# Optimization experiments

Hardware: AMD Instinct MI355X
Metric: run time of the kernel (lower is better)

The kernel has to match this reference:

```python
import jax, jax.numpy as jnp
import numpy as np

H, KVH, HD, D, FF = 16, 4, 128, 2048, 7168
EPS = 1e-5
ROPE_THETA = 10000.0
SCALE_FACTOR, SCALE_GAP = 1.0, 0.7


def rms_norm(x, w):
    v = jnp.mean(jnp.square(x.astype(jnp.float32)), axis=-1, keepdims=True)
    return (x.astype(jnp.float32) * jax.lax.rsqrt(v + EPS)).astype(x.dtype) * w


def apply_rope(x, pos):
    # x: [B,S,h,HD], pos: [S]
    inv = 1.0 / (ROPE_THETA ** (jnp.arange(0, HD, 2, dtype=jnp.float32) / HD))
    ang = pos.astype(jnp.float32)[:, None] * inv[None, :]              # [S,HD/2]
    cos = jnp.concatenate([jnp.cos(ang)] * 2, -1)[None, :, None, :]    # [1,S,1,HD]
    sin = jnp.concatenate([jnp.sin(ang)] * 2, -1)[None, :, None, :]
    x1, x2 = jnp.split(x, 2, axis=-1)
    rot = jnp.concatenate([-x2, x1], axis=-1)
    return x * cos + rot * sin


def attention(x, q_w, k_w, v_w, o_w):
    B, S, _ = x.shape
    pos = jnp.arange(S)
    q = apply_rope((x @ q_w.T).reshape(B, S, H, HD), pos)
    k = apply_rope((x @ k_w.T).reshape(B, S, KVH, HD), pos)
    v = (x @ v_w.T).reshape(B, S, KVH, HD)
    rep = H // KVH
    k = jnp.repeat(k, rep, axis=2)   # [B,S,H,HD]
    v = jnp.repeat(v, rep, axis=2)
    scores = jnp.einsum('bqhd,bkhd->bhqk', q, k) / np.sqrt(HD).astype(np.float32)
    causal = jnp.tril(jnp.ones((S, S), dtype=bool))
    scores = jnp.where(causal[None, None], scores, jnp.finfo(scores.dtype).min)
    probs = jax.nn.softmax(scores, axis=-1)
    out = jnp.einsum('bhqk,bkhd->bqhd', probs, v).reshape(B, S, H * HD)
    return out @ o_w.T


def mlp(x, gate_w, up_w, down_w):
    return (jax.nn.silu(x @ gate_w.T) * (x @ up_w.T)) @ down_w.T


def setup_inputs() -> dict:
    key = jax.random.key(0)
    ks = jax.random.split(key, 12)
    B, S = 2, 2048
    w = lambda k, shp: (jax.random.normal(k, shp, dtype=jnp.float32) * 0.02)
    return {
        'hidden_states': jax.random.normal(ks[0], (B, S, D), dtype=jnp.float32),
        'topk_mask': jax.random.randint(ks[1], (B, S), 0, 2) > 0,
        'topk_scores': jax.random.uniform(ks[2], (B, S), dtype=jnp.float32),
        'ln1_w': jnp.ones((D,), jnp.float32),
        'ln2_w': jnp.ones((D,), jnp.float32),
        'q_w': w(ks[3], (H * HD, D)),
        'k_w': w(ks[4], (KVH * HD, D)),
        'v_w': w(ks[5], (KVH * HD, D)),
        'o_w': w(ks[6], (D, H * HD)),
        'gate_w': w(ks[7], (FF, D)),
        'up_w': w(ks[8], (FF, D)),
        'down_w': w(ks[9], (D, FF)),
    }


def reference(hidden_states, topk_mask, topk_scores, ln1_w, ln2_w,
              q_w, k_w, v_w, o_w, gate_w, up_w, down_w):
    # attention block
    h = hidden_states + attention(rms_norm(hidden_states, ln1_w), q_w, k_w, v_w, o_w)
    # MoD top-k masked MLP: only selected tokens go through MLP, scaled, scattered back
    m = mlp(rms_norm(h, ln2_w), gate_w, up_w, down_w)
    scores = 0.5 * SCALE_FACTOR + (topk_scores - 0.5) * SCALE_GAP
    upd = jnp.where(topk_mask[..., None], m * scores[..., None], 0.0)
    return h + upd
```

## Files before the change

kernel.cpp:

```cpp
#include <hip/hip_runtime.h>
#include <stdint.h>

#define SEQ    2048
#define DMODEL 2048
#define NTOK   4096
#define NHEAD  16
#define NKVH   4
#define HDIM   128
#define FFDIM  7168
#define FFH    3584
#define QKVS   3072

typedef __bf16 bf16x8 __attribute__((ext_vector_type(8)));
typedef float  floatx4 __attribute__((ext_vector_type(4)));

__device__ __forceinline__ float bf2f(unsigned short u) {
  union { unsigned int i; float f; } v; v.i = ((unsigned int)u) << 16; return v.f;
}
__device__ __forceinline__ unsigned short f2bf(float f) {
  union { float f; unsigned int u; } v; v.f = f;
  unsigned int r = (v.u + 0x7FFFu + ((v.u >> 16) & 1u)) >> 16;
  return (unsigned short)r;
}
__device__ __forceinline__ uint4 ld8f32(const float* p) {
  float4 a = *(const float4*)p, b = *(const float4*)(p + 4);
  union { unsigned short s[8]; uint4 v; } o;
  o.s[0] = f2bf(a.x); o.s[1] = f2bf(a.y); o.s[2] = f2bf(a.z); o.s[3] = f2bf(a.w);
  o.s[4] = f2bf(b.x); o.s[5] = f2bf(b.y); o.s[6] = f2bf(b.z); o.s[7] = f2bf(b.w);
  return o.v;
}

__device__ __forceinline__ void gload16(const unsigned short* g, unsigned short* l) {
  __builtin_amdgcn_global_load_lds(
      (const __attribute__((address_space(1))) unsigned int*)g,
      (__attribute__((address_space(3))) unsigned int*)l, 16, 0, 0);
}

__global__ __launch_bounds__(256) void wconv_attn(
    const float* __restrict__ q, const float* __restrict__ k,
    const float* __restrict__ v, const float* __restrict__ o,
    unsigned short* __restrict__ wqkv, unsigned short* __restrict__ wo,
    int* __restrict__ cnt) {
  if (blockIdx.x == 0 && threadIdx.x == 0) *cnt = 0;
  const int r = blockIdx.x;
  const float* src;
  unsigned short* dst;
  if (r < 2048)      { src = q + (size_t)r * DMODEL;          dst = wqkv + (size_t)r * DMODEL; }
  else if (r < 2560) { src = k + (size_t)(r - 2048) * DMODEL; dst = wqkv + (size_t)r * DMODEL; }
  else if (r < 3072) { src = v + (size_t)(r - 2560) * DMODEL; dst = wqkv + (size_t)r * DMODEL; }
  else               { src = o + (size_t)(r - 3072) * DMODEL; dst = wo + (size_t)(r - 3072) * DMODEL; }
  const int c = threadIdx.x * 8;
  *(uint4*)(dst + c) = ld8f32(src + c);
}

__global__ __launch_bounds__(256) void wconv_gu(
    const float* __restrict__ g, const float* __restrict__ u,
    unsigned short* __restrict__ dst, int hf) {
  const int r = blockIdx.x;
  const float* src = (r < FFH) ? g + ((size_t)hf * FFH + r) * DMODEL
                               : u + ((size_t)hf * FFH + (r - FFH)) * DMODEL;
  const int c = threadIdx.x * 8;
  *(uint4*)(dst + (size_t)r * DMODEL + c) = ld8f32(src + c);
}

__global__ __launch_bounds__(256) void wconv_dn(const float* __restrict__ s,
                                                unsigned short* __restrict__ d, int koff) {
  const int r = blockIdx.x;
  const float* sp = s + (size_t)r * FFDIM + koff;
  unsigned short* dp = d + (size_t)r * FFH;
  for (int c = threadIdx.x * 8; c < FFH; c += 2048)
    *(uint4*)(dp + c) = ld8f32(sp + c);
}

#define GEMM_CORE_G(Aptr, Wptr, LDA, LDB, KLEN, KOFF)                            \
  __shared__ __align__(16) unsigned short As[128 * 32];                          \
  __shared__ __align__(16) unsigned short Bs[128 * 32];                          \
  const int tid  = threadIdx.x;                                                  \
  const int wave = tid >> 6, lane = tid & 63;                                    \
  const int quad = lane >> 4, l16 = lane & 15;                                   \
  const int row0 = blockIdx.y * 128, col0 = blockIdx.x * 128;                    \
  const int wm = (wave >> 1) * 64, wn = (wave & 1) * 64;                         \
  const floatx4 z = {0.f, 0.f, 0.f, 0.f};                                       \
  floatx4 acc[4][4];                                                             \
  _Pragma("unroll") for (int i = 0; i < 4; ++i)                                  \
  _Pragma("unroll") for (int j = 0; j < 4; ++j) acc[i][j] = z;                   \
  const int ar0 = tid >> 2, ac0 = (tid & 3) << 3;                                \
  unsigned short* lA0 = &As[wave * 512];                                         \
  unsigned short* lA1 = &As[2048 + wave * 512];                                  \
  unsigned short* lB0 = &Bs[wave * 512];                                         \
  unsigned short* lB1 = &Bs[2048 + wave * 512];                                  \
  const unsigned short* gA0 = (Aptr) + (size_t)(row0 + ar0) * (LDA) + (KOFF) + ac0;      \
  const unsigned short* gA1 = (Aptr) + (size_t)(row0 + 64 + ar0) * (LDA) + (KOFF) + ac0; \
  const unsigned short* gB0 = (Wptr) + (size_t)(col0 + ar0) * (LDB) + (KOFF) + ac0;      \
  const unsigned short* gB1 = (Wptr) + (size_t)(col0 + 64 + ar0) * (LDB) + (KOFF) + ac0; \
  for (int k0 = 0; k0 < (KLEN); k0 += 32) {                                      \
    gload16(gA0 + k0, lA0);                                                      \
    gload16(gA1 + k0, lA1);                                                      \
    gload16(gB0 + k0, lB0);                                                      \
    gload16(gB1 + k0, lB1);                                                      \
    __syncthreads();                                                             \
    bf16x8 af[4], bfr[4];                                                        \
    _Pragma("unroll") for (int i = 0; i < 4; ++i) {                              \
      af[i]  = *(const bf16x8*)&As[(wm + i * 16 + l16) * 32 + quad * 8];         \
      bfr[i] = *(const bf16x8*)&Bs[(wn + i * 16 + l16) * 32 + quad * 8];         \
    }                                                                            \
    _Pragma("unroll") for (int mi = 0; mi < 4; ++mi)                             \
    _Pragma("unroll") for (int ni = 0; ni < 4; ++ni)                             \
      acc[mi][ni] =                                                              \
          __builtin_amdgcn_mfma_f32_16x16x32_bf16(af[mi], bfr[ni], acc[mi][ni], 0, 0, 0); \
    __syncthreads();                                                             \
  }

__global__ __launch_bounds__(256) void gemm_bt(
    const unsigned short* __restrict__ A, const unsigned short* __restrict__ W,
    unsigned short* __restrict__ C, int N, int K) {
  GEMM_CORE_G(A, W, K, K, K, 0)
#pragma unroll
  for (int mi = 0; mi < 4; ++mi) {
    const int r = row0 + wm + mi * 16 + quad * 4;
#pragma unroll
    for (int ni = 0; ni < 4; ++ni) {
      const int cc = col0 + wn + ni * 16 + l16;
#pragma unroll
      for (int reg = 0; reg < 4; ++reg)
        C[(size_t)(r + reg) * N + cc] = f2bf(acc[mi][ni][reg]);
    }
  }
}

__global__ __launch_bounds__(256) void gemm_o_res(
    const unsigned short* __restrict__ A, const unsigned short* __restrict__ W,
    const float* __restrict__ X, float* __restrict__ Hout) {
  GEMM_CORE_G(A, W, DMODEL, DMODEL, DMODEL, 0)
#pragma unroll
  for (int mi = 0; mi < 4; ++mi) {
    const int r = row0 + wm + mi * 16 + quad * 4;
#pragma unroll
    for (int ni = 0; ni < 4; ++ni) {
      const int cc = col0 + wn + ni * 16 + l16;
#pragma unroll
      for (int reg = 0; reg < 4; ++reg) {
        const size_t idx = (size_t)(r + reg) * DMODEL + cc;
        Hout[idx] = X[idx] + acc[mi][ni][reg];
      }
    }
  }
}

__global__ __launch_bounds__(256) void gemm_down_add(
    const unsigned short* __restrict__ A, const unsigned short* __restrict__ W,
    const float* __restrict__ ts, const int* __restrict__ tok_of,
    const int* __restrict__ cnt, float* __restrict__ out) {
  const int nrow = *cnt;
  if (blockIdx.y * 128 >= nrow) return;
  const int koff = blockIdx.z * (FFH / 2);
  GEMM_CORE_G(A, W, FFH, FFH, FFH / 2, koff)
#pragma unroll
  for (int mi = 0; mi < 4; ++mi) {
    const int r = row0 + wm + mi * 16 + quad * 4;
#pragma unroll
    for (int ni = 0; ni < 4; ++ni) {
      const int cc = col0 + wn + ni * 16 + l16;
#pragma unroll
      for (int reg = 0; reg < 4; ++reg) {
        const int rr = r + reg;
        if (rr < nrow) {
          const int tok = tok_of[rr];
          const float scv = 0.5f + (ts[tok] - 0.5f) * 0.7f;
          atomicAdd(out + (size_t)tok * DMODEL + cc, acc[mi][ni][reg] * scv);
        }
      }
    }
  }
}

__global__ __launch_bounds__(256) void gemm_gateup(
    const unsigned short* __restrict__ A, const unsigned short* __restrict__ G,
    const unsigned short* __restrict__ U, const int* __restrict__ cnt,
    unsigned short* __restrict__ act) {
  if (blockIdx.y * 128 >= *cnt) return;
  __shared__ __align__(16) unsigned short As[128 * 32];
  __shared__ __align__(16) unsigned short Gs[64 * 32];
  __shared__ __align__(16) unsigned short Us[64 * 32];
  const int tid  = threadIdx.x;
  const int wave = tid >> 6, lane = tid & 63;
  const int quad = lane >> 4, l16 = lane & 15;
  const int row0 = blockIdx.y * 128, colg = blockIdx.x * 64;
  const int wm = (wave >> 1) * 64, wn = (wave & 1) * 32;

  const floatx4 z = {0.f, 0.f, 0.f, 0.f};
  floatx4 accG[4][2], accU[4][2];
#pragma unroll
  for (int i = 0; i < 4; ++i)
#pragma unroll
    for (int j = 0; j < 2; ++j) { accG[i][j] = z; accU[i][j] = z; }

  const int ar0 = tid >> 2, ac0 = (tid & 3) << 3;
  unsigned short* lA0 = &As[wave * 512];
  unsigned short* lA1 = &As[2048 + wave * 512];
  unsigned short* lG  = &Gs[wave * 512];
  unsigned short* lU  = &Us[wave * 512];
  const unsigned short* gA0 = A + (size_t)(row0 + ar0) * DMODEL + ac0;
  const unsigned short* gA1 = A + (size_t)(row0 + 64 + ar0) * DMODEL + ac0;
  const unsigned short* gG  = G + (size_t)(colg + ar0) * DMODEL + ac0;
  const unsigned short* gU  = U + (size_t)(colg + ar0) * DMODEL + ac0;

  for (int k0 = 0; k0 < DMODEL; k0 += 32) {
    gload16(gA0 + k0, lA0);
    gload16(gA1 + k0, lA1);
    gload16(gG + k0, lG);
    gload16(gU + k0, lU);
    __syncthreads();
    bf16x8 af[4], bg[2], bu[2];
#pragma unroll
    for (int i = 0; i < 4; ++i)
      af[i] = *(const bf16x8*)&As[(wm + i * 16 + l16) * 32 + quad * 8];
#pragma unroll
    for (int j = 0; j < 2; ++j) {
      bg[j] = *(const bf16x8*)&Gs[(wn + j * 16 + l16) * 32 + quad * 8];
      bu[j] = *(const bf16x8*)&Us[(wn + j * 16 + l16) * 32 + quad * 8];
    }
#pragma unroll
    for (int mi = 0; mi < 4; ++mi)
#pragma unroll
      for (int ni = 0; ni < 2; ++ni) {
        accG[mi][ni] = __builtin_amdgcn_mfma_f32_16x16x32_bf16(af[mi], bg[ni], accG[mi][ni], 0, 0, 0);
        accU[mi][ni] = __builtin_amdgcn_mfma_f32_16x16x32_bf16(af[mi], bu[ni], accU[mi][ni], 0, 0, 0);
      }
    __syncthreads();
  }
#pragma unroll
  for (int mi = 0; mi < 4; ++mi) {
    const int r = row0 + wm + mi * 16 + quad * 4;
#pragma unroll
    for (int ni = 0; ni < 2; ++ni) {
      const int cc = colg + wn + ni * 16 + l16;
#pragma unroll
      for (int reg = 0; reg < 4; ++reg) {
        const float g = accG[mi][ni][reg];
        const float u = accU[mi][ni][reg];
        const float s = g / (1.f + __expf(-g));
        act[(size_t)(r + reg) * FFH + cc] = f2bf(s * u);
      }
    }
  }
}

__global__ __launch_bounds__(256) void rmsnorm_f32(
    const float* __restrict__ x, const float* __restrict__ w,
    unsigned short* __restrict__ out) {
  __shared__ float red[4];
  const int row = blockIdx.x, tid = threadIdx.x;
  const int lane = tid & 63, wave = tid >> 6;
  const size_t base = (size_t)row * DMODEL + tid * 8;
  float4 a = *(const float4*)(x + base);
  float4 b = *(const float4*)(x + base + 4);
  float v[8] = {a.x, a.y, a.z, a.w, b.x, b.y, b.z, b.w};
  float ss = 0.f;
#pragma unroll
  for (int j = 0; j < 8; ++j) ss += v[j] * v[j];
#pragma unroll
  for (int off = 32; off; off >>= 1) ss += __shfl_xor(ss, off);
  if (lane == 0) red[wave] = ss;
  __syncthreads();
  const float tot = red[0] + red[1] + red[2] + red[3];
  const float rms = rsqrtf(tot * (1.f / (float)DMODEL) + 1e-5f);
  float4 wa = *(const float4*)(w + tid * 8);
  float4 wb = *(const float4*)(w + tid * 8 + 4);
  const float wv[8] = {wa.x, wa.y, wa.z, wa.w, wb.x, wb.y, wb.z, wb.w};
  unsigned short o[8];
#pragma unroll
  for (int j = 0; j < 8; ++j) o[j] = f2bf(v[j] * rms * wv[j]);
  *(uint4*)(out + base) = *(const uint4*)o;
}

__global__ __launch_bounds__(256) void rms_gather(
    const float* __restrict__ x, const float* __restrict__ w,
    const int* __restrict__ mask, int* __restrict__ cnt,
    int* __restrict__ tok_of, unsigned short* __restrict__ xc) {
  const int row = blockIdx.x;
  if (!mask[row]) return;
  __shared__ float red[4];
  __shared__ int ppos;
  const int tid = threadIdx.x, lane = tid & 63, wave = tid >> 6;
  if (tid == 0) { const int p = atomicAdd(cnt, 1); ppos = p; tok_of[p] = row; }
  const size_t base = (size_t)row * DMODEL + tid * 8;
  float4 a = *(const float4*)(x + base);
  float4 b = *(const float4*)(x + base + 4);
  float v[8] = {a.x, a.y, a.z, a.w, b.x, b.y, b.z, b.w};
  float ss = 0.f;
#pragma unroll
  for (int j = 0; j < 8; ++j) ss += v[j] * v[j];
#pragma unroll
  for (int off = 32; off; off >>= 1) ss += __shfl_xor(ss, off);
  if (lane == 0) red[wave] = ss;
  __syncthreads();
  const float tot = red[0] + red[1] + red[2] + red[3];
  const float rms = rsqrtf(tot * (1.f / (float)DMODEL) + 1e-5f);
  float4 wa = *(const float4*)(w + tid * 8);
  float4 wb = *(const float4*)(w + tid * 8 + 4);
  const float wv[8] = {wa.x, wa.y, wa.z, wa.w, wb.x, wb.y, wb.z, wb.w};
  unsigned short o[8];
#pragma unroll
  for (int j = 0; j < 8; ++j) o[j] = f2bf(v[j] * rms * wv[j]);
  *(uint4*)(xc + (size_t)ppos * DMODEL + tid * 8) = *(const uint4*)o;
}

__global__ __launch_bounds__(256) void rope_k(unsigned short* __restrict__ buf,
                                              int nh, int rstride) {
  const int t = blockIdx.x;
  const int s = t & (SEQ - 1);
  const int d = threadIdx.x & 63;
  const float inv = __expf((float)d * -0.14391156843712787f);
  float sn, cs;
  __sincosf((float)s * inv, &sn, &cs);
  const int npair = nh * 64;
  for (int idx = threadIdx.x; idx < npair; idx += 256) {
    const int hh = idx >> 6;
    unsigned short* p = buf + (size_t)t * rstride + hh * 128 + d;
    const float x1 = bf2f(p[0]), x2 = bf2f(p[64]);
    p[0]  = f2bf(x1 * cs - x2 * sn);
    p[64] = f2bf(x2 * cs + x1 * sn);
  }
}

__global__ __launch_bounds__(512, 2) void attn(
    const unsigned short* __restrict__ QKV,
    unsigned short* __restrict__ O) {
  __shared__ __align__(16) unsigned short Ks[64 * 136];
  __shared__ __align__(16) unsigned short Vt[128 * 80];
  __shared__ __align__(16) unsigned short Ps[8][16 * 88];
  const int h = blockIdx.x, b = blockIdx.z;
  const int qtL = blockIdx.y, qtH = 15 - qtL;
  const int kvh = h >> 2;
  const int tid = threadIdx.x, wave = tid >> 6, lane = tid & 63;
  const int quad = lane >> 4, l16 = lane & 15;
  const int wloH = qtH * 128 + wave * 16;
  const int wloL = qtL * 128 + wave * 16;
  const int qrH = wloH + quad * 4, qrL = wloL + quad * 4;
  const float sscale = 0.08838834764831845f;

  bf16x8 qfH[4], qfL[4];
  {
    const unsigned short* qpH =
        QKV + (size_t)(b * SEQ + wloH + l16) * QKVS + h * HDIM + quad * 8;
    const unsigned short* qpL =
        QKV + (size_t)(b * SEQ + wloL + l16) * QKVS + h * HDIM + quad * 8;
#pragma unroll
    for (int c = 0; c < 4; ++c) {
      qfH[c] = *(const bf16x8*)(qpH + 32 * c);
      qfL[c] = *(const bf16x8*)(qpL + 32 * c);
    }
  }
  const floatx4 z = {0.f, 0.f, 0.f, 0.f};
  floatx4 accH[8], accL[8];
#pragma unroll
  for (int i = 0; i < 8; ++i) { accH[i] = z; accL[i] = z; }
  float mH[4], lH[4], mL[4], lL[4];
#pragma unroll
  for (int r = 0; r < 4; ++r) { mH[r] = -1e30f; lH[r] = 0.f; mL[r] = -1e30f; lL[r] = 0.f; }

  const int sr = tid >> 4, scol = (tid & 15) * 8;
  const unsigned short* kvb = QKV + (size_t)(b * SEQ) * QKVS + kvh * HDIM;
  uint4 kreg[2], vreg[2];

  auto LOADT = [&](int t0) {
#pragma unroll
    for (int it = 0; it < 2; ++it) {
      const int r = sr + it * 32;
      kreg[it] = *(const uint4*)(kvb + (size_t)(t0 + r) * QKVS + 2048 + scol);
      vreg[it] = *(const uint4*)(kvb + (size_t)(t0 + r) * QKVS + 2560 + scol);
    }
  };
  auto STORET = [&]() {
#pragma unroll
    for (int it = 0; it < 2; ++it) {
      const int r = sr + it * 32;
      *(uint4*)&Ks[r * 136 + scol] = kreg[it];
      const unsigned short* dv = (const unsigned short*)&vreg[it];
      const int tb = r >> 3, pos = r & 7;
#pragma unroll
      for (int j = 0; j < 8; ++j) {
        const int d = scol + j;
        const int sb = tb ^ ((d >> 3) & 7);
        Vt[d * 80 + sb * 8 + pos] = dv[j];
      }
    }
  };

  auto COMPUTE = [&](const bf16x8* qf, floatx4* accO, float* mrow, float* lrow,
                     int qrowC, int wlo, int t0) {
    floatx4 sc[4];
    __builtin_amdgcn_s_setprio(1);
#pragma unroll
    for (int ni = 0; ni < 4; ++ni) {
      floatx4 s = z;
#pragma unroll
      for (int c = 0; c < 4; ++c) {
        bf16x8 kf = *(const bf16x8*)&Ks[(ni * 16 + l16) * 136 + c * 32 + quad * 8];
        s = __builtin_amdgcn_mfma_f32_16x16x32_bf16(qf[c], kf, s, 0, 0, 0);
      }
      sc[ni] = s;
    }
    __builtin_amdgcn_s_setprio(0);

    if (t0 + 63 > wlo) {
#pragma unroll
      for (int ni = 0; ni < 4; ++ni) {
        const int kcol = t0 + ni * 16 + l16;
#pragma unroll
        for (int reg = 0; reg < 4; ++reg) {
          const float vv = sc[ni][reg] * sscale;
          sc[ni][reg] = (kcol > qrowC + reg) ? -1e30f : vv;
        }
      }
    } else {
#pragma unroll
      for (int ni = 0; ni < 4; ++ni)
#pragma unroll
        for (int reg = 0; reg < 4; ++reg) sc[ni][reg] *= sscale;
    }

    float mx[4];
#pragma unroll
    for (int reg = 0; reg < 4; ++reg) {
      float m0 = fmaxf(fmaxf(sc[0][reg], sc[1][reg]), fmaxf(sc[2][reg], sc[3][reg]));
#pragma unroll
      for (int off = 1; off < 16; off <<= 1) m0 = fmaxf(m0, __shfl_xor(m0, off));
      mx[reg] = m0;
    }
    const bool grow = (mx[0] > mrow[0] + 8.f) || (mx[1] > mrow[1] + 8.f) ||
                      (mx[2] > mrow[2] + 8.f) || (mx[3] > mrow[3] + 8.f);
    if (__any(grow)) {
#pragma unroll
      for (int reg = 0; reg < 4; ++reg) {
        const float mnew = fmaxf(mrow[reg], mx[reg]);
        const float alpha = __expf(mrow[reg] - mnew);
        mrow[reg] = mnew;
        lrow[reg] *= alpha;
#pragma unroll
        for (int nd = 0; nd < 8; ++nd) accO[nd][reg] *= alpha;
      }
    }
#pragma unroll
    for (int reg = 0; reg < 4; ++reg) {
      float rs = 0.f;
#pragma unroll
      for (int ni = 0; ni < 4; ++ni) {
        const float p = __expf(sc[ni][reg] - mrow[reg]);
        sc[ni][reg] = p;
        rs += p;
      }
#pragma unroll
      for (int off = 1; off < 16; off <<= 1) rs += __shfl_xor(rs, off);
      lrow[reg] += rs;
    }
#pragma unroll
    for (int ni = 0; ni < 4; ++ni)
#pragma unroll
      for (int reg = 0; reg < 4; ++reg)
        Ps[wave][(quad * 4 + reg) * 88 + ni * 16 + l16] = f2bf(sc[ni][reg]);
    const bf16x8 pa0 = *(const bf16x8*)&Ps[wave][l16 * 88 + quad * 8];
    const bf16x8 pa1 = *(const bf16x8*)&Ps[wave][l16 * 88 + 32 + quad * 8];
    __builtin_amdgcn_s_setprio(1);
#pragma unroll
    for (int nd = 0; nd < 8; ++nd) {
      const int d = nd * 16 + l16;
      const int f = (d >> 3) & 7;
      bf16x8 v0 = *(const bf16x8*)&Vt[d * 80 + ((quad ^ f) << 3)];
      bf16x8 v1 = *(const bf16x8*)&Vt[d * 80 + (((quad + 4) ^ f) << 3)];
      accO[nd] = __builtin_amdgcn_mfma_f32_16x16x32_bf16(pa0, v0, accO[nd], 0, 0, 0);
      accO[nd] = __builtin_amdgcn_mfma_f32_16x16x32_bf16(pa1, v1, accO[nd], 0, 0, 0);
    }
    __builtin_amdgcn_s_setprio(0);
  };

  const int ntL = 2 * qtL + 2, ntH = 2 * qtH + 2;
  LOADT(0);
  STORET();
  __syncthreads();

  for (int ti = 0; ti < ntH; ++ti) {
    const int t0 = ti * 64;
    const bool more = (ti + 1 < ntH);
    if (more) LOADT(t0 + 64);

    if (t0 <= wloH + 15) COMPUTE(qfH, accH, mH, lH, qrH, wloH, t0);
    if (ti < ntL && t0 <= wloL + 15) COMPUTE(qfL, accL, mL, lL, qrL, wloL, t0);

    __syncthreads();
    if (more) {
      STORET();
      __syncthreads();
    }
  }
#pragma unroll
  for (int nd = 0; nd < 8; ++nd)
#pragma unroll
    for (int reg = 0; reg < 4; ++reg) {
      const float oH = accH[nd][reg] / lH[reg];
      O[(size_t)(b * SEQ + qrH + reg) * (NHEAD * HDIM) + h * HDIM + nd * 16 + l16] = f2bf(oH);
      const float oL = accL[nd][reg] / lL[reg];
      O[(size_t)(b * SEQ + qrL + reg) * (NHEAD * HDIM) + h * HDIM + nd * 16 + l16] = f2bf(oL);
    }
}

extern "C" void kernel_launch(void* const* d_in, const int* in_sizes, int n_in,
                              void* d_out, int out_size, void* d_ws, size_t ws_size,
                              hipStream_t stream) {
  (void)in_sizes; (void)n_in; (void)out_size; (void)ws_size;
  const float* x    = (const float*)d_in[0];
  const int*   mask = (const int*)d_in[1];
  const float* ts   = (const float*)d_in[2];
  const float* ln1  = (const float*)d_in[3];
  const float* ln2  = (const float*)d_in[4];
  const float* q_w  = (const float*)d_in[5];
  const float* k_w  = (const float*)d_in[6];
  const float* v_w  = (const float*)d_in[7];
  const float* o_w  = (const float*)d_in[8];
  const float* g_w  = (const float*)d_in[9];
  const float* u_w  = (const float*)d_in[10];
  const float* dn_w = (const float*)d_in[11];
  float* out = (float*)d_out;

  char* ws = (char*)d_ws;
  unsigned short* xn    = (unsigned short*)(ws + 0);
  unsigned short* qkv   = (unsigned short*)(ws + 16777216);
  unsigned short* wqkv  = (unsigned short*)(ws + 41943040);
  unsigned short* attno = (unsigned short*)(ws + 41943040);
  unsigned short* wo    = (unsigned short*)(ws + 58720256);
  unsigned short* xc    = (unsigned short*)(ws + 0);
  unsigned short* wg    = (unsigned short*)(ws + 16777216);
  unsigned short* wu    = (unsigned short*)(ws + 31457280);
  unsigned short* wdn   = (unsigned short*)(ws + 16777216);
  unsigned short* act   = (unsigned short*)(ws + 46137344);
  int*            cnt   = (int*)           (ws + 75497472);
  int*            tok_of= (int*)           (ws + 75501568);

  wconv_attn<<<5120, 256, 0, stream>>>(q_w, k_w, v_w, o_w, wqkv, wo, cnt);
  rmsnorm_f32<<<NTOK, 256, 0, stream>>>(x, ln1, xn);
  gemm_bt<<<dim3(QKVS / 128, 32), 256, 0, stream>>>(xn, wqkv, qkv, QKVS, 2048);
  rope_k<<<NTOK, 256, 0, stream>>>(qkv, 20, QKVS);
  attn<<<dim3(NHEAD, 8, 2), 512, 0, stream>>>(qkv, attno);
  gemm_o_res<<<dim3(16, 32), 256, 0, stream>>>(attno, wo, x, out);

  rms_gather<<<NTOK, 256, 0, stream>>>(out, ln2, mask, cnt, tok_of, xc);
  for (int hf = 0; hf < 2; ++hf) {
    wconv_gu<<<2 * FFH, 256, 0, stream>>>(g_w, u_w, wg, hf);
    gemm_gateup<<<dim3(FFH / 64, 32), 256, 0, stream>>>(xc, wg, wu, cnt, act);
    wconv_dn<<<2048, 256, 0, stream>>>(dn_w, wdn, hf * FFH);
    gemm_down_add<<<dim3(16, 32, 2), 256, 0, stream>>>(act, wdn, ts, tok_of, cnt, out);
  }
}
```

Measured before the change: 906.9 us.

## Convert down-proj weights once upfront and interleave high/low query tiles in attention

The down-projection weight conversion now happens once, inside the initial attention-weight conversion kernel, into a dedicated workspace region. This removes two per-half conversion launches, and the down GEMM indexes the full-width buffer with the larger leading dimension. The attention kernel now computes the paired high and low query tiles together in a single loop body, sharing each K/V fragment load across both MFMA chains, and it reloads the low-tile Q fragments from global memory each iteration to save registers. The trade-offs are more workspace, a larger up-front conversion, repeated Q loads and a bigger register footprint.

```diff
diff --git a/kernel.cpp b/kernel.cpp
--- a/kernel.cpp
+++ b/kernel.cpp
@@ -39,18 +39,27 @@
 __global__ __launch_bounds__(256) void wconv_attn(
     const float* __restrict__ q, const float* __restrict__ k,
     const float* __restrict__ v, const float* __restrict__ o,
+    const float* __restrict__ dn,
     unsigned short* __restrict__ wqkv, unsigned short* __restrict__ wo,
-    int* __restrict__ cnt) {
+    unsigned short* __restrict__ wdn, int* __restrict__ cnt) {
   if (blockIdx.x == 0 && threadIdx.x == 0) *cnt = 0;
   const int r = blockIdx.x;
-  const float* src;
-  unsigned short* dst;
-  if (r < 2048)      { src = q + (size_t)r * DMODEL;          dst = wqkv + (size_t)r * DMODEL; }
-  else if (r < 2560) { src = k + (size_t)(r - 2048) * DMODEL; dst = wqkv + (size_t)r * DMODEL; }
-  else if (r < 3072) { src = v + (size_t)(r - 2560) * DMODEL; dst = wqkv + (size_t)r * DMODEL; }
-  else               { src = o + (size_t)(r - 3072) * DMODEL; dst = wo + (size_t)(r - 3072) * DMODEL; }
-  const int c = threadIdx.x * 8;
-  *(uint4*)(dst + c) = ld8f32(src + c);
+  if (r < 5120) {
+    const float* src;
+    unsigned short* dst;
+    if (r < 2048)      { src = q + (size_t)r * DMODEL;          dst = wqkv + (size_t)r * DMODEL; }
+    else if (r < 2560) { src = k + (size_t)(r - 2048) * DMODEL; dst = wqkv + (size_t)r * DMODEL; }
+    else if (r < 3072) { src = v + (size_t)(r - 2560) * DMODEL; dst = wqkv + (size_t)r * DMODEL; }
+    else               { src = o + (size_t)(r - 3072) * DMODEL; dst = wo + (size_t)(r - 3072) * DMODEL; }
+    const int c = threadIdx.x * 8;
+    *(uint4*)(dst + c) = ld8f32(src + c);
+  } else {
+    const int rr = r - 5120;
+    const float* sp = dn + (size_t)rr * FFDIM;
+    unsigned short* dp = wdn + (size_t)rr * FFDIM;
+    for (int c = threadIdx.x * 8; c < FFDIM; c += 2048)
+      *(uint4*)(dp + c) = ld8f32(sp + c);
+  }
 }
 
 __global__ __launch_bounds__(256) void wconv_gu(
@@ -61,15 +70,6 @@
                                : u + ((size_t)hf * FFH + (r - FFH)) * DMODEL;
   const int c = threadIdx.x * 8;
   *(uint4*)(dst + (size_t)r * DMODEL + c) = ld8f32(src + c);
-}
-
-__global__ __launch_bounds__(256) void wconv_dn(const float* __restrict__ s,
-                                                unsigned short* __restrict__ d, int koff) {
-  const int r = blockIdx.x;
-  const float* sp = s + (size_t)r * FFDIM + koff;
-  unsigned short* dp = d + (size_t)r * FFH;
-  for (int c = threadIdx.x * 8; c < FFH; c += 2048)
-    *(uint4*)(dp + c) = ld8f32(sp + c);
 }
 
 #define GEMM_CORE_G(Aptr, Wptr, LDA, LDB, KLEN, KOFF)                            \
@@ -154,7 +154,7 @@
   const int nrow = *cnt;
   if (blockIdx.y * 128 >= nrow) return;
   const int koff = blockIdx.z * (FFH / 2);
-  GEMM_CORE_G(A, W, FFH, FFH, FFH / 2, koff)
+  GEMM_CORE_G(A, W, FFH, FFDIM, FFH / 2, koff)
 #pragma unroll
   for (int mi = 0; mi < 4; ++mi) {
     const int r = row0 + wm + mi * 16 + quad * 4;
@@ -340,17 +340,14 @@
   const int qrH = wloH + quad * 4, qrL = wloL + quad * 4;
   const float sscale = 0.08838834764831845f;
 
-  bf16x8 qfH[4], qfL[4];
+  const unsigned short* qpL =
+      QKV + (size_t)(b * SEQ + wloL + l16) * QKVS + h * HDIM + quad * 8;
+  bf16x8 qfH[4];
   {
     const unsigned short* qpH =
         QKV + (size_t)(b * SEQ + wloH + l16) * QKVS + h * HDIM + quad * 8;
-    const unsigned short* qpL =
-        QKV + (size_t)(b * SEQ + wloL + l16) * QKVS + h * HDIM + quad * 8;
-#pragma unroll
-    for (int c = 0; c < 4; ++c) {
-      qfH[c] = *(const bf16x8*)(qpH + 32 * c);
-      qfL[c] = *(const bf16x8*)(qpL + 32 * c);
-    }
+#pragma unroll
+    for (int c = 0; c < 4; ++c) qfH[c] = *(const bf16x8*)(qpH + 32 * c);
   }
   const floatx4 z = {0.f, 0.f, 0.f, 0.f};
   floatx4 accH[8], accL[8];
@@ -388,39 +385,8 @@
     }
   };
 
-  auto COMPUTE = [&](const bf16x8* qf, floatx4* accO, float* mrow, float* lrow,
-                     int qrowC, int wlo, int t0) {
-    floatx4 sc[4];
-    __builtin_amdgcn_s_setprio(1);
-#pragma unroll
-    for (int ni = 0; ni < 4; ++ni) {
-      floatx4 s = z;
-#pragma unroll
-      for (int c = 0; c < 4; ++c) {
-        bf16x8 kf = *(const bf16x8*)&Ks[(ni * 16 + l16) * 136 + c * 32 + quad * 8];
-        s = __builtin_amdgcn_mfma_f32_16x16x32_bf16(qf[c], kf, s, 0, 0, 0);
-      }
-      sc[ni] = s;
-    }
-    __builtin_amdgcn_s_setprio(0);
-
-    if (t0 + 63 > wlo) {
-#pragma unroll
-      for (int ni = 0; ni < 4; ++ni) {
-        const int kcol = t0 + ni * 16 + l16;
-#pragma unroll
-        for (int reg = 0; reg < 4; ++reg) {
-          const float vv = sc[ni][reg] * sscale;
-          sc[ni][reg] = (kcol > qrowC + reg) ? -1e30f : vv;
-        }
-      }
-    } else {
-#pragma unroll
-      for (int ni = 0; ni < 4; ++ni)
-#pragma unroll
-        for (int reg = 0; reg < 4; ++reg) sc[ni][reg] *= sscale;
-    }
-
+  auto SOFTPA = [&](floatx4* sc, float* mrow, float* lrow, floatx4* accO,
+                    bf16x8& pa0, bf16x8& pa1) {
     float mx[4];
 #pragma unroll
     for (int reg = 0; reg < 4; ++reg) {
@@ -460,19 +426,8 @@
 #pragma unroll
       for (int reg = 0; reg < 4; ++reg)
         Ps[wave][(quad * 4 + reg) * 88 + ni * 16 + l16] = f2bf(sc[ni][reg]);
-    const bf16x8 pa0 = *(const bf16x8*)&Ps[wave][l16 * 88 + quad * 8];
-    const bf16x8 pa1 = *(const bf16x8*)&Ps[wave][l16 * 88 + 32 + quad * 8];
-    __builtin_amdgcn_s_setprio(1);
-#pragma unroll
-    for (int nd = 0; nd < 8; ++nd) {
-      const int d = nd * 16 + l16;
-      const int f = (d >> 3) & 7;
-      bf16x8 v0 = *(const bf16x8*)&Vt[d * 80 + ((quad ^ f) << 3)];
-      bf16x8 v1 = *(const bf16x8*)&Vt[d * 80 + (((quad + 4) ^ f) << 3)];
-      accO[nd] = __builtin_amdgcn_mfma_f32_16x16x32_bf16(pa0, v0, accO[nd], 0, 0, 0);
-      accO[nd] = __builtin_amdgcn_mfma_f32_16x16x32_bf16(pa1, v1, accO[nd], 0, 0, 0);
-    }
-    __builtin_amdgcn_s_setprio(0);
+    pa0 = *(const bf16x8*)&Ps[wave][l16 * 88 + quad * 8];
+    pa1 = *(const bf16x8*)&Ps[wave][l16 * 88 + 32 + quad * 8];
   };
 
   const int ntL = 2 * qtL + 2, ntH = 2 * qtH + 2;
@@ -485,8 +440,107 @@
     const bool more = (ti + 1 < ntH);
     if (more) LOADT(t0 + 64);
 
-    if (t0 <= wloH + 15) COMPUTE(qfH, accH, mH, lH, qrH, wloH, t0);
-    if (ti < ntL && t0 <= wloL + 15) COMPUTE(qfL, accL, mL, lL, qrL, wloL, t0);
+    const bool aH = (t0 <= wloH + 15);
+    const bool aL = (ti < ntL) && (t0 <= wloL + 15);
+
+    if (aL) {
+      bf16x8 qfLt[4];
+#pragma unroll
+      for (int c = 0; c < 4; ++c) qfLt[c] = *(const bf16x8*)(qpL + 32 * c);
+      floatx4 sH[4], sL[4];
+      __builtin_amdgcn_s_setprio(1);
+#pragma unroll
+      for (int ni = 0; ni < 4; ++ni) {
+        floatx4 a = z, bb = z;
+#pragma unroll
+        for (int c = 0; c < 4; ++c) {
+          bf16x8 kf = *(const bf16x8*)&Ks[(ni * 16 + l16) * 136 + c * 32 + quad * 8];
+          a  = __builtin_amdgcn_mfma_f32_16x16x32_bf16(qfH[c], kf, a, 0, 0, 0);
+          bb = __builtin_amdgcn_mfma_f32_16x16x32_bf16(qfLt[c], kf, bb, 0, 0, 0);
+        }
+        sH[ni] = a; sL[ni] = bb;
+      }
+      __builtin_amdgcn_s_setprio(0);
+#pragma unroll
+      for (int ni = 0; ni < 4; ++ni)
+#pragma unroll
+        for (int reg = 0; reg < 4; ++reg) sH[ni][reg] *= sscale;
+      if (t0 + 63 > wloL) {
+#pragma unroll
+        for (int ni = 0; ni < 4; ++ni) {
+          const int kcol = t0 + ni * 16 + l16;
+#pragma unroll
+          for (int reg = 0; reg < 4; ++reg) {
+            const float vv = sL[ni][reg] * sscale;
+            sL[ni][reg] = (kcol > qrL + reg) ? -1e30f : vv;
+          }
+        }
+      } else {
+#pragma unroll
+        for (int ni = 0; ni < 4; ++ni)
+#pragma unroll
+          for (int reg = 0; reg < 4; ++reg) sL[ni][reg] *= sscale;
+      }
+      bf16x8 paH0, paH1, paL0, paL1;
+      SOFTPA(sH, mH, lH, accH, paH0, paH1);
+      SOFTPA(sL, mL, lL, accL, paL0, paL1);
+      __builtin_amdgcn_s_setprio(1);
+#pragma unroll
+      for (int nd = 0; nd < 8; ++nd) {
+        const int d = nd * 16 + l16;
+        const int f = (d >> 3) & 7;
+        bf16x8 v0 = *(const bf16x8*)&Vt[d * 80 + ((quad ^ f) << 3)];
+        bf16x8 v1 = *(const bf16x8*)&Vt[d * 80 + (((quad + 4) ^ f) << 3)];
+        accH[nd] = __builtin_amdgcn_mfma_f32_16x16x32_bf16(paH0, v0, accH[nd], 0, 0, 0);
+        accH[nd] = __builtin_amdgcn_mfma_f32_16x16x32_bf16(paH1, v1, accH[nd], 0, 0, 0);
+        accL[nd] = __builtin_amdgcn_mfma_f32_16x16x32_bf16(paL0, v0, accL[nd], 0, 0, 0);
+        accL[nd] = __builtin_amdgcn_mfma_f32_16x16x32_bf16(paL1, v1, accL[nd], 0, 0, 0);
+      }
+      __builtin_amdgcn_s_setprio(0);
+    } else if (aH) {
+      floatx4 sc[4];
+      __builtin_amdgcn_s_setprio(1);
+#pragma unroll
+      for (int ni = 0; ni < 4; ++ni) {
+        floatx4 s = z;
+#pragma unroll
+        for (int c = 0; c < 4; ++c) {
+          bf16x8 kf = *(const bf16x8*)&Ks[(ni * 16 + l16) * 136 + c * 32 + quad * 8];
+          s = __builtin_amdgcn_mfma_f32_16x16x32_bf16(qfH[c], kf, s, 0, 0, 0);
+        }
+        sc[ni] = s;
+      }
+      __builtin_amdgcn_s_setprio(0);
+      if (t0 + 63 > wloH) {
+#pragma unroll
+        for (int ni = 0; ni < 4; ++ni) {
+          const int kcol = t0 + ni * 16 + l16;
+#pragma unroll
+          for (int reg = 0; reg < 4; ++reg) {
+            const float vv = sc[ni][reg] * sscale;
+            sc[ni][reg] = (kcol > qrH + reg) ? -1e30f : vv;
+          }
+        }
+      } else {
+#pragma unroll
+        for (int ni = 0; ni < 4; ++ni)
+#pragma unroll
+          for (int reg = 0; reg < 4; ++reg) sc[ni][reg] *= sscale;
+      }
+      bf16x8 pa0, pa1;
+      SOFTPA(sc, mH, lH, accH, pa0, pa1);
+      __builtin_amdgcn_s_setprio(1);
+#pragma unroll
+      for (int nd = 0; nd < 8; ++nd) {
+        const int d = nd * 16 + l16;
+        const int f = (d >> 3) & 7;
+        bf16x8 v0 = *(const bf16x8*)&Vt[d * 80 + ((quad ^ f) << 3)];
+        bf16x8 v1 = *(const bf16x8*)&Vt[d * 80 + (((quad + 4) ^ f) << 3)];
+        accH[nd] = __builtin_amdgcn_mfma_f32_16x16x32_bf16(pa0, v0, accH[nd], 0, 0, 0);
+        accH[nd] = __builtin_amdgcn_mfma_f32_16x16x32_bf16(pa1, v1, accH[nd], 0, 0, 0);
+      }
+      __builtin_amdgcn_s_setprio(0);
+    }
 
     __syncthreads();
     if (more) {
@@ -532,12 +586,12 @@
   unsigned short* xc    = (unsigned short*)(ws + 0);
   unsigned short* wg    = (unsigned short*)(ws + 16777216);
   unsigned short* wu    = (unsigned short*)(ws + 31457280);
-  unsigned short* wdn   = (unsigned short*)(ws + 16777216);
   unsigned short* act   = (unsigned short*)(ws + 46137344);
-  int*            cnt   = (int*)           (ws + 75497472);
-  int*            tok_of= (int*)           (ws + 75501568);
-
-  wconv_attn<<<5120, 256, 0, stream>>>(q_w, k_w, v_w, o_w, wqkv, wo, cnt);
+  unsigned short* wdn   = (unsigned short*)(ws + 75497472);
+  int*            cnt   = (int*)           (ws + 104857600);
+  int*            tok_of= (int*)           (ws + 104857608);
+
+  wconv_attn<<<7168, 256, 0, stream>>>(q_w, k_w, v_w, o_w, dn_w, wqkv, wo, wdn, cnt);
   rmsnorm_f32<<<NTOK, 256, 0, stream>>>(x, ln1, xn);
   gemm_bt<<<dim3(QKVS / 128, 32), 256, 0, stream>>>(xn, wqkv, qkv, QKVS, 2048);
   rope_k<<<NTOK, 256, 0, stream>>>(qkv, 20, QKVS);
@@ -548,7 +602,7 @@
   for (int hf = 0; hf < 2; ++hf) {
     wconv_gu<<<2 * FFH, 256, 0, stream>>>(g_w, u_w, wg, hf);
     gemm_gateup<<<dim3(FFH / 64, 32), 256, 0, stream>>>(xc, wg, wu, cnt, act);
-    wconv_dn<<<2048, 256, 0, stream>>>(dn_w, wdn, hf * FFH);
-    gemm_down_add<<<dim3(16, 32, 2), 256, 0, stream>>>(act, wdn, ts, tok_of, cnt, out);
-  }
-}
+    gemm_down_add<<<dim3(16, 32, 2), 256, 0, stream>>>(act, wdn + (size_t)hf * FFH,
+                                                       ts, tok_of, cnt, out);
+  }
+}
```

Result: no change. 892.5 us (-1.6%).
